# Performance work log

Hardware: AMD Instinct MI355X
Metric: run time of the kernel (lower is better)

Reference implementation:

```python
import jax, jax.numpy as jnp
import numpy as np

EPS = 1e-5
GROUPS = 8

def group_norm(x, gamma, beta):
    # x: [B,C,H,W], 8 groups
    B, C, H, W = x.shape
    xg = x.reshape(B, GROUPS, C // GROUPS, H, W)
    mu = jnp.mean(xg, axis=(2, 3, 4), keepdims=True)
    var = jnp.mean((xg - mu) ** 2, axis=(2, 3, 4), keepdims=True)
    xn = ((xg - mu) * jax.lax.rsqrt(var + EPS)).reshape(B, C, H, W)
    return xn * gamma[None, :, None, None] + beta[None, :, None, None]

def setup_inputs() -> dict:
    key = jax.random.key(0)
    ks = jax.random.split(key, 7)
    B, C, H, W = 4, 256, 64, 64
    x = jax.random.normal(ks[0], (B, C, H, W), dtype=jnp.float32)
    gamma = jnp.ones((C,), dtype=jnp.float32)
    beta = jnp.zeros((C,), dtype=jnp.float32)
    s = 1.0 / np.sqrt(C)
    w_qkv = jax.random.normal(ks[1], (3 * C, C), dtype=jnp.float32) * s
    b_qkv = jnp.zeros((3 * C,), dtype=jnp.float32)
    w_proj = jax.random.normal(ks[2], (C, C), dtype=jnp.float32) * s
    b_proj = jnp.zeros((C,), dtype=jnp.float32)
    return {"x": x, "gamma": gamma, "beta": beta, "w_qkv": w_qkv,
            "b_qkv": b_qkv, "w_proj": w_proj, "b_proj": b_proj}

def reference(x, gamma, beta, w_qkv, b_qkv, w_proj, b_proj):
    B, C, H, W = x.shape
    N = H * W
    h = group_norm(x, gamma, beta)
    # 1x1 conv == per-pixel matmul
    qkv = jnp.einsum('bchw,oc->bohw', h, w_qkv) + b_qkv[None, :, None, None]
    q, k, v = jnp.split(qkv, 3, axis=1)  # each [B,C,H,W]
    q = q.reshape(B, C, N).transpose(0, 2, 1)   # [B,N,C]
    k = k.reshape(B, C, N)                      # [B,C,N]
    v = v.reshape(B, C, N).transpose(0, 2, 1)   # [B,N,C]
    attn = jax.nn.softmax(jnp.einsum('bnc,bcm->bnm', q, k) / jnp.sqrt(jnp.float32(C)), axis=-1)
    out = jnp.einsum('bnm,bmc->bnc', attn, v)   # [B,N,C]
    out = out.transpose(0, 2, 1).reshape(B, C, H, W)
    proj = jnp.einsum('bchw,oc->bohw', out, w_proj) + b_proj[None, :, None, None]
    return x + proj
```

## Files before the change

### kernel.cpp

```cpp
#include <hip/hip_runtime.h>
#include <hip/hip_bf16.h>
#include <math.h>

#define B 4
#define C 256
#define G 8
#define N 4096
#define EPSV 1e-5f
#define QSCALE 0.0901684400f
#define THR2 11.5416f

typedef __attribute__((ext_vector_type(8))) short short8;
typedef __attribute__((ext_vector_type(16))) float f32x16;
typedef unsigned short ushort_t;
typedef unsigned int uint_t;

__device__ __forceinline__ ushort_t f2bf(float f) {
    union { float f; uint_t u; } c; c.f = f;
    uint_t u = c.u;
    uint_t r = (u + 0x7FFFu + ((u >> 16) & 1u)) >> 16;
    return (ushort_t)r;
}
__device__ __forceinline__ float bf2f(ushort_t h) {
    union { uint_t u; float f; } c; c.u = ((uint_t)h) << 16;
    return c.f;
}
__device__ __forceinline__ uint_t pack2(float a, float b) {
    return (uint_t)f2bf(a) | ((uint_t)f2bf(b) << 16);
}
__device__ __forceinline__ uint_t cvtpk_bf16(float lo, float hi) {
    uint_t r;
    asm("v_cvt_pk_bf16_f32 %0, %1, %2" : "=v"(r) : "v"(lo), "v"(hi));
    return r;
}
__device__ __forceinline__ float fexp2(float x) {
    return __builtin_amdgcn_exp2f(x);
}
__device__ __forceinline__ void gl_lds16(const void* g, void* l) {
    __builtin_amdgcn_global_load_lds(
        (const __attribute__((address_space(1))) void*)g,
        (__attribute__((address_space(3))) void*)l, 16, 0, 0);
}

__global__ __launch_bounds__(256) void gn_wconv(const float* __restrict__ x,
        float* __restrict__ partials, const float* __restrict__ wq,
        const float* __restrict__ wp, ushort_t* __restrict__ wbf) {
    int blk = blockIdx.x;
    if (blk < 256) {
        int bg = blk >> 3;
        int part = blk & 7;
        const float4* xp4 = (const float4*)(x + (size_t)bg * (32 * N) + (size_t)part * (32 * N / 8));
        float s = 0.f, ss = 0.f;
        for (int i = threadIdx.x; i < 4096; i += 256) {
            float4 v = xp4[i];
            s  += v.x + v.y + v.z + v.w;
            ss += v.x*v.x + v.y*v.y + v.z*v.z + v.w*v.w;
        }
        __shared__ float rs[256], rss[256];
        rs[threadIdx.x] = s; rss[threadIdx.x] = ss;
        __syncthreads();
        for (int off = 128; off > 0; off >>= 1) {
            if (threadIdx.x < off) {
                rs[threadIdx.x]  += rs[threadIdx.x + off];
                rss[threadIdx.x] += rss[threadIdx.x + off];
            }
            __syncthreads();
        }
        if (threadIdx.x == 0) {
            partials[(bg*8 + part)*2]     = rs[0];
            partials[(bg*8 + part)*2 + 1] = rss[0];
        }
    } else {
        int idx = (blk - 256)*256 + threadIdx.x;
        #pragma unroll
        for (int p = 0; p < 4; p++) {
            int id = idx + p*16384;
            float4 v = (id < 49152) ? ((const float4*)wq)[id] : ((const float4*)wp)[id - 49152];
            uint2 pk; pk.x = pack2(v.x, v.y); pk.y = pack2(v.z, v.w);
            *(uint2*)&wbf[(size_t)id*4] = pk;
        }
    }
}

__global__ __launch_bounds__(256) void qkv_fused(const float* __restrict__ x,
        const ushort_t* __restrict__ wbf, const float* __restrict__ gamma,
        const float* __restrict__ beta, const float* __restrict__ partials,
        const float* __restrict__ bias,
        ushort_t* __restrict__ qbf, ushort_t* __restrict__ kimg, ushort_t* __restrict__ vimg) {
    int b = blockIdx.z, o0 = blockIdx.y*64, n0 = blockIdx.x*128;
    int tid = threadIdx.x;
    int w = tid>>6, l = tid&63, l31 = l&31, lh = l>>5;
    int cg = tid >> 5;
    int nq = tid & 31;
    __shared__ short Ws[2][4096];
    __shared__ short Hs[2][8192];
    __shared__ float sst[16];

    if (tid < 8) {
        float s = 0.f, ss = 0.f;
        #pragma unroll
        for (int p = 0; p < 8; p++) {
            s  += partials[((b*8 + tid)*8 + p)*2];
            ss += partials[((b*8 + tid)*8 + p)*2 + 1];
        }
        const float inv = 1.f / 131072.f;
        float mu = s * inv;
        float var = fmaxf(ss * inv - mu*mu, 0.f);
        sst[tid*2]     = mu;
        sst[tid*2 + 1] = rsqrtf(var + EPSV);
    }
    __syncthreads();

    const ushort_t* wb = wbf + (size_t)o0*256;

    auto stageW = [&](int bb, int c0) {
        #pragma unroll
        for (int q = 0; q < 2; q++) {
            int u0 = q*256 + w*64;
            int u  = u0 + l;
            int row = u & 63, ch = u >> 6;
            gl_lds16(wb + (size_t)row*256 + c0 + ch*8, &Ws[bb][u0*8]);
        }
    };
    auto loadX = [&](int c0, float4* xv) {
        const float* xb = x + ((size_t)b*C + c0 + cg*8)*N + n0 + nq*4;
        #pragma unroll
        for (int e = 0; e < 8; e++)
            xv[e] = *(const float4*)(xb + (size_t)e*N);
    };
    auto writeH = [&](int bb, int c0, const float4* xv) {
        int cbase = c0 + cg*8;
        int g = cbase >> 5;
        float mu = sst[g*2], rs = sst[g*2+1];
        float ga[8], be[8];
        #pragma unroll
        for (int e = 0; e < 8; e++) {
            float gm = gamma[cbase+e];
            ga[e] = gm*rs;
            be[e] = beta[cbase+e] - mu*ga[e];
        }
        #pragma unroll
        for (int j = 0; j < 4; j++) {
            float h[8];
            #pragma unroll
            for (int e = 0; e < 8; e++) {
                float vx = (j==0) ? xv[e].x : (j==1) ? xv[e].y : (j==2) ? xv[e].z : xv[e].w;
                h[e] = vx*ga[e] + be[e];
            }
            uint4 pk;
            pk.x = pack2(h[0], h[1]);
            pk.y = pack2(h[2], h[3]);
            pk.z = pack2(h[4], h[5]);
            pk.w = pack2(h[6], h[7]);
            *(uint4*)&Hs[bb][(size_t)(cg*128 + nq*4 + j)*8] = pk;
        }
    };

    int wo = w & 1;
    int wn = w >> 1;
    f32x16 acc[2];
    #pragma unroll
    for (int nf = 0; nf < 2; nf++)
        #pragma unroll
        for (int r = 0; r < 16; r++) acc[nf][r] = 0.f;

    float4 xv[8];
    loadX(0, xv);
    stageW(0, 0);
    writeH(0, 0, xv);
    __syncthreads();

    for (int t = 0; t < 4; t++) {
        int bb = t & 1;
        if (t < 3) { stageW(bb^1, (t+1)*64); loadX((t+1)*64, xv); }
        short8 af[4];
        #pragma unroll
        for (int s = 0; s < 4; s++)
            af[s] = *(const short8*)&Ws[bb][((2*s+lh)*64 + wo*32 + l31)*8];
        #pragma unroll
        for (int nf = 0; nf < 2; nf++) {
            int nfr = wn*2 + nf;
            #pragma unroll
            for (int s = 0; s < 4; s++) {
                short8 hf = *(const short8*)&Hs[bb][((2*s+lh)*128 + nfr*32 + l31)*8];
                acc[nf] = __builtin_amdgcn_mfma_f32_32x32x16_bf16(af[s], hf, acc[nf], 0, 0, 0);
            }
        }
        if (t < 3) writeH(bb^1, (t+1)*64, xv);
        __syncthreads();
    }

    int ow = o0 + wo*32;
    float bv[16];
    #pragma unroll
    for (int r = 0; r < 16; r++) bv[r] = bias[ow + (r&3) + 8*(r>>2) + 4*lh];

    if (ow < 256) {
        #pragma unroll
        for (int nf = 0; nf < 2; nf++) {
            int n = n0 + (wn*2 + nf)*32 + l31;
            ushort_t* row = qbf + ((size_t)(b*N + n))*256 + ow;
            #pragma unroll
            for (int rp = 0; rp < 8; rp++) {
                int r0 = rp*2;
                int cl = (r0&3) + 8*(r0>>2) + 4*lh;
                uint_t wd = cvtpk_bf16((acc[nf][r0]+bv[r0])*QSCALE, (acc[nf][r0+1]+bv[r0+1])*QSCALE);
                *(uint_t*)(row + cl) = wd;
            }
        }
    } else if (ow < 512) {
        int cb = ow - 256;
        #pragma unroll
        for (int nf = 0; nf < 2; nf++) {
            int n = n0 + (wn*2 + nf)*32 + l31;
            ushort_t* tbase = kimg + (size_t)b*1048576 + (size_t)(n>>5)*8192
                            + (size_t)l31*8 + 4*lh;
            #pragma unroll
            for (int g = 0; g < 4; g++) {
                uint2 pk;
                pk.x = pack2(acc[nf][g*4+0]+bv[g*4+0], acc[nf][g*4+1]+bv[g*4+1]);
                pk.y = pack2(acc[nf][g*4+2]+bv[g*4+2], acc[nf][g*4+3]+bv[g*4+3]);
                *(uint2*)(tbase + (size_t)((cb>>3)+g)*256) = pk;
            }
        }
    } else {
        int cb = ow - 512;
        #pragma unroll
        for (int nf = 0; nf < 2; nf++) {
            int n = n0 + (wn*2 + nf)*32 + l31;
            ushort_t* tbase = vimg + (size_t)b*1048576 + (size_t)(n>>5)*8192
                            + (size_t)(l31>>3)*2048 + (l31&7);
            #pragma unroll
            for (int r = 0; r < 16; r++) {
                int cl = (r&3) + 8*(r>>2) + 4*lh;
                tbase[(size_t)(cb+cl)*8] = f2bf(acc[nf][r] + bv[r]);
            }
        }
    }
}

__global__ __launch_bounds__(256, 2) void attn_mfma(const ushort_t* __restrict__ qbf,
        const ushort_t* __restrict__ kimg, const ushort_t* __restrict__ vimg,
        ushort_t* __restrict__ part, float* __restrict__ ml) {
    int f = blockIdx.x;
    int comb = f & 15;
    int qt  = f >> 4;
    int b   = comb >> 2;
    int kvq = comb & 3;
    constexpr int NT = 32;
    int w = threadIdx.x >> 6;
    int l = threadIdx.x & 63;
    int l31 = l & 31, lh = l >> 5;

    __shared__ short KV[2][2][8192];

    int qbase = qt*128 + w*32;
    short8 qf[16];
    {
        const ushort_t* qrow = qbf + ((size_t)(b*N + qbase + l31))*256;
        #pragma unroll
        for (int s = 0; s < 16; s++)
            qf[s] = *(const short8*)(qrow + s*16 + lh*8);
    }

    f32x16 ot[8];
    #pragma unroll
    for (int mc = 0; mc < 8; mc++)
        #pragma unroll
        for (int r = 0; r < 16; r++) ot[mc][r] = 0.f;
    float m = -INFINITY, lsum = 0.f;

    const char* kbase = (const char*)kimg + (size_t)b*2097152;
    const char* vbase = (const char*)vimg + (size_t)b*2097152;

    auto stage = [&](int slot, int t) {
        int tile = kvq*32 + t;
        const char* kt = kbase + (size_t)tile*16384;
        const char* vt = vbase + (size_t)tile*16384;
        #pragma unroll
        for (int q = 0; q < 4; q++) {
            int u0 = (w*4 + q)*64;
            gl_lds16(kt + (u0 + l)*16, &KV[slot][0][u0*8]);
            gl_lds16(vt + (u0 + l)*16, &KV[slot][1][u0*8]);
        }
    };

    stage(0, 0);

    for (int t = 0; t < NT; t++) {
        int slot = t & 1;
        __syncthreads();
        if (t+1 < NT) stage(slot^1, t+1);

        f32x16 st0, st1;
        #pragma unroll
        for (int r = 0; r < 16; r++) { st0[r] = 0.f; st1[r] = 0.f; }
        const short* kb_ = &KV[slot][0][0];
        __builtin_amdgcn_s_setprio(1);
        #pragma unroll
        for (int s = 0; s < 8; s++) {
            short8 ka = *(const short8*)(kb_ + ((size_t)((4*s   + lh)*32 + l31))*8);
            short8 kc = *(const short8*)(kb_ + ((size_t)((4*s+2 + lh)*32 + l31))*8);
            st0 = __builtin_amdgcn_mfma_f32_32x32x16_bf16(ka, qf[2*s],   st0, 0, 0, 0);
            st1 = __builtin_amdgcn_mfma_f32_32x32x16_bf16(kc, qf[2*s+1], st1, 0, 0, 0);
        }
        __builtin_amdgcn_s_setprio(0);

        float sv[16];
        #pragma unroll
        for (int r = 0; r < 16; r++) sv[r] = st0[r] + st1[r];

        float a0 = fmaxf(sv[0], sv[1]),  a1 = fmaxf(sv[2], sv[3]);
        float a2 = fmaxf(sv[4], sv[5]),  a3 = fmaxf(sv[6], sv[7]);
        float a4 = fmaxf(sv[8], sv[9]),  a5 = fmaxf(sv[10], sv[11]);
        float a6 = fmaxf(sv[12], sv[13]), a7 = fmaxf(sv[14], sv[15]);
        float b0 = fmaxf(a0, a1), b1 = fmaxf(a2, a3), b2 = fmaxf(a4, a5), b3 = fmaxf(a6, a7);
        float pmax = fmaxf(fmaxf(b0, b1), fmaxf(b2, b3));
        pmax = fmaxf(pmax, __shfl_xor(pmax, 32));
        if (!__all(pmax <= m + THR2)) {
            float mn = fmaxf(m, pmax);
            float fac = fexp2(m - mn);
            m = mn;
            lsum *= fac;
            #pragma unroll
            for (int mc = 0; mc < 8; mc++)
                #pragma unroll
                for (int r = 0; r < 16; r++) ot[mc][r] *= fac;
        }
        float p[16];
        #pragma unroll
        for (int r = 0; r < 16; r++) p[r] = fexp2(sv[r] - m);
        float s0_ = (p[0]+p[1]) + (p[2]+p[3]);
        float s1_ = (p[4]+p[5]) + (p[6]+p[7]);
        float s2_ = (p[8]+p[9]) + (p[10]+p[11]);
        float s3_ = (p[12]+p[13]) + (p[14]+p[15]);
        float ls = (s0_+s1_) + (s2_+s3_);
        ls += __shfl_xor(ls, 32);
        lsum += ls;

        short8 pf0, pf1;
        {
            uint_t x0 = cvtpk_bf16(p[0], p[1]);
            uint_t y0 = cvtpk_bf16(p[4], p[5]);
            uint_t x1 = cvtpk_bf16(p[2], p[3]);
            uint_t y1 = cvtpk_bf16(p[6], p[7]);
            auto r0 = __builtin_amdgcn_permlane32_swap(x0, y0, false, false);
            auto r1 = __builtin_amdgcn_permlane32_swap(x1, y1, false, false);
            union { uint_t u[4]; short8 s8; } u_;
            u_.u[0] = r0[0]; u_.u[1] = r1[0]; u_.u[2] = r0[1]; u_.u[3] = r1[1];
            pf0 = u_.s8;
            uint_t x2 = cvtpk_bf16(p[8],  p[9]);
            uint_t y2 = cvtpk_bf16(p[12], p[13]);
            uint_t x3 = cvtpk_bf16(p[10], p[11]);
            uint_t y3 = cvtpk_bf16(p[14], p[15]);
            auto r2 = __builtin_amdgcn_permlane32_swap(x2, y2, false, false);
            auto r3 = __builtin_amdgcn_permlane32_swap(x3, y3, false, false);
            union { uint_t u[4]; short8 s8; } u2_;
            u2_.u[0] = r2[0]; u2_.u[1] = r3[0]; u2_.u[2] = r2[1]; u2_.u[3] = r3[1];
            pf1 = u2_.s8;
        }

        const short* vb_ = &KV[slot][1][0];
        __builtin_amdgcn_s_setprio(1);
        #pragma unroll
        for (int mc = 0; mc < 8; mc++) {
            short8 v0 = *(const short8*)(vb_ + ((size_t)((lh)*256   + mc*32 + l31))*8);
            short8 v1 = *(const short8*)(vb_ + ((size_t)((2+lh)*256 + mc*32 + l31))*8);
            ot[mc] = __builtin_amdgcn_mfma_f32_32x32x16_bf16(v0, pf0, ot[mc], 0, 0, 0);
            ot[mc] = __builtin_amdgcn_mfma_f32_32x32x16_bf16(v1, pf1, ot[mc], 0, 0, 0);
        }
        __builtin_amdgcn_s_setprio(0);
    }

    float invl = 1.f / lsum;
    ushort_t* pbase = part + (size_t)kvq*4194304 + ((size_t)(b*N + qbase + l31))*256;
    #pragma unroll
    for (int mc = 0; mc < 8; mc++)
        #pragma unroll
        for (int rp = 0; rp < 8; rp++) {
            int r0 = rp*2;
            uint_t wd = cvtpk_bf16(ot[mc][r0]*invl, ot[mc][r0+1]*invl);
            int c0 = (r0 & 3) + 8*(r0 >> 2) + 4*lh + 32*mc;
            *(uint_t*)(pbase + c0) = wd;
        }
    if (l < 32) {
        size_t row = (size_t)kvq*16384 + b*4096 + qbase + l;
        ml[row*2]     = m;
        ml[row*2 + 1] = lsum;
    }
}

__global__ __launch_bounds__(256) void proj_merge(const ushort_t* __restrict__ part,
        const float* __restrict__ ml, const ushort_t* __restrict__ wpbf,
        const float* __restrict__ bp, const float* __restrict__ x, float* __restrict__ out) {
    int b = blockIdx.z, o0 = blockIdx.y*128, n0 = blockIdx.x*64;
    int tid = threadIdx.x;
    int w = tid>>6, l = tid&63, l31 = l&31, lh = l>>5;
    __shared__ short Ws[2][8192];
    __shared__ short Hs[2][4096];

    const ushort_t* wb = wpbf + (size_t)o0*256;

    int srow = tid & 63;
    int ch0  = tid >> 6;
    size_t rowbase = ((size_t)(b*4096 + n0 + srow))*256;
    float wv[4];
    {
        float mv[4], lv[4];
        #pragma unroll
        for (int i = 0; i < 4; i++) {
            size_t rr = (size_t)i*16384 + b*4096 + n0 + srow;
            mv[i] = ml[rr*2];
            lv[i] = ml[rr*2 + 1];
        }
        float M = fmaxf(fmaxf(mv[0], mv[1]), fmaxf(mv[2], mv[3]));
        float wsum = 0.f;
        #pragma unroll
        for (int i = 0; i < 4; i++) { wv[i] = fexp2(mv[i] - M)*lv[i]; wsum += wv[i]; }
        float inv = 1.f / wsum;
        #pragma unroll
        for (int i = 0; i < 4; i++) wv[i] *= inv;
    }

    auto stageW = [&](int bb, int c0) {
        #pragma unroll
        for (int q = 0; q < 4; q++) {
            int u0 = (q*4 + w)*64;
            int u  = u0 + l;
            int row = u & 127, ch = u >> 7;
            gl_lds16(wb + (size_t)row*256 + c0 + ch*8, &Ws[bb][u0*8]);
        }
    };
    short8 hA[4], hB[4];
    auto Hload = [&](int c0) {
        #pragma unroll
        for (int i = 0; i < 4; i++) {
            const ushort_t* pp = part + (size_t)i*4194304 + rowbase + c0;
            hA[i] = *(const short8*)(pp + ch0*8);
            hB[i] = *(const short8*)(pp + (ch0+4)*8);
        }
    };
    auto Hwrite = [&](int bb) {
        float oA[8], oB[8];
        #pragma unroll
        for (int e = 0; e < 8; e++) { oA[e] = 0.f; oB[e] = 0.f; }
        #pragma unroll
        for (int i = 0; i < 4; i++) {
            float wi = wv[i];
            #pragma unroll
            for (int e = 0; e < 8; e++) {
                oA[e] += wi*bf2f((ushort_t)hA[i][e]);
                oB[e] += wi*bf2f((ushort_t)hB[i][e]);
            }
        }
        uint4 pkA, pkB;
        pkA.x = pack2(oA[0], oA[1]); pkA.y = pack2(oA[2], oA[3]);
        pkA.z = pack2(oA[4], oA[5]); pkA.w = pack2(oA[6], oA[7]);
        pkB.x = pack2(oB[0], oB[1]); pkB.y = pack2(oB[2], oB[3]);
        pkB.z = pack2(oB[4], oB[5]); pkB.w = pack2(oB[6], oB[7]);
        *(uint4*)&Hs[bb][(size_t)(ch0*64 + srow)*8]     = pkA;
        *(uint4*)&Hs[bb][(size_t)((ch0+4)*64 + srow)*8] = pkB;
    };

    f32x16 acc[2];
    #pragma unroll
    for (int nf = 0; nf < 2; nf++)
        #pragma unroll
        for (int r = 0; r < 16; r++) acc[nf][r] = 0.f;

    stageW(0, 0);
    Hload(0);
    Hwrite(0);
    __syncthreads();
    for (int t = 0; t < 4; t++) {
        int bb = t & 1;
        if (t < 3) { stageW(bb^1, (t+1)*64); Hload((t+1)*64); }
        short8 af[4];
        #pragma unroll
        for (int s = 0; s < 4; s++)
            af[s] = *(const short8*)&Ws[bb][((2*s+lh)*128 + w*32 + l31)*8];
        #pragma unroll
        for (int nf = 0; nf < 2; nf++) {
            #pragma unroll
            for (int s = 0; s < 4; s++) {
                short8 hf = *(const short8*)&Hs[bb][((2*s+lh)*64 + nf*32 + l31)*8];
                acc[nf] = __builtin_amdgcn_mfma_f32_32x32x16_bf16(af[s], hf, acc[nf], 0, 0, 0);
            }
        }
        if (t < 3) Hwrite(bb^1);
        __syncthreads();
    }

    int cw = o0 + w*32;
    float bv[16];
    #pragma unroll
    for (int r = 0; r < 16; r++) bv[r] = bp[cw + (r&3) + 8*(r>>2) + 4*lh];

    #pragma unroll
    for (int nf = 0; nf < 2; nf++) {
        int n = n0 + nf*32 + l31;
        #pragma unroll
        for (int r = 0; r < 16; r++) {
            int cl = (r&3) + 8*(r>>2) + 4*lh;
            size_t a = ((size_t)b*C + cw + cl)*N + n;
            out[a] = acc[nf][r] + bv[r] + x[a];
        }
    }
}

extern "C" void kernel_launch(void* const* d_in, const int* in_sizes, int n_in,
                              void* d_out, int out_size, void* d_ws, size_t ws_size,
                              hipStream_t stream) {
    const float* x      = (const float*)d_in[0];
    const float* gamma  = (const float*)d_in[1];
    const float* beta   = (const float*)d_in[2];
    const float* w_qkv  = (const float*)d_in[3];
    const float* b_qkv  = (const float*)d_in[4];
    const float* w_proj = (const float*)d_in[5];
    const float* b_proj = (const float*)d_in[6];
    float* out = (float*)d_out;
    char* wsb  = (char*)d_ws;

    const size_t MB = 1048576;
    ushort_t* qbf  = (ushort_t*)(wsb);
    ushort_t* kimg = (ushort_t*)(wsb + 8*MB);
    ushort_t* vimg = (ushort_t*)(wsb + 16*MB);
    ushort_t* part = (ushort_t*)(wsb + 24*MB);
    float*    ml   = (float*)  (wsb + 56*MB);
    float* partials = (float*) (wsb + 56*MB + 524288);
    ushort_t* wbf  = (ushort_t*)(wsb + 56*MB + 528384);

    gn_wconv<<<dim3(320), dim3(256), 0, stream>>>(x, partials, w_qkv, w_proj, wbf);
    qkv_fused<<<dim3(32, 12, 4), dim3(256), 0, stream>>>(x, wbf, gamma, beta, partials, b_qkv, qbf, kimg, vimg);
    attn_mfma<<<dim3(512), dim3(256), 0, stream>>>(qbf, kimg, vimg, part, ml);
    proj_merge<<<dim3(64, 2, 4), dim3(256), 0, stream>>>(part, ml, wbf + 196608, b_proj, x, out);
}
```

Before: 137.7 us.

## Software-pipeline attention: issue next QK^T before softmax, triple-buffer V

Restructures the flash-attention loop so the QK^T MFMAs for tile t+1 are issued right after the PV MFMAs of tile t. The softmax of tile t+1 then overlaps with matrix work, and K/V loads are prefetched two tiles ahead. LDS is split into a double-buffered K and a triple-buffered V, and the separate p[] array is folded into sv[] to save registers. This raises LDS use per block and may increase register pressure under launch_bounds(256,2). The new barrier placement also needs the buffer indexing to stay race-free.

```diff
diff --git a/kernel.cpp b/kernel.cpp
--- a/kernel.cpp
+++ b/kernel.cpp
@@ -252,7 +252,8 @@
     int l = threadIdx.x & 63;
     int l31 = l & 31, lh = l >> 5;
 
-    __shared__ short KV[2][2][8192];
+    __shared__ short Kl[2][8192];
+    __shared__ short Vl[3][8192];
 
     int qbase = qt*128 + w*32;
     short8 qf[16];
@@ -273,29 +274,25 @@
     const char* kbase = (const char*)kimg + (size_t)b*2097152;
     const char* vbase = (const char*)vimg + (size_t)b*2097152;
 
-    auto stage = [&](int slot, int t) {
-        int tile = kvq*32 + t;
+    auto stage = [&](int j) {
+        int tile = kvq*32 + j;
         const char* kt = kbase + (size_t)tile*16384;
         const char* vt = vbase + (size_t)tile*16384;
+        short* kd = &Kl[j & 1][0];
+        short* vd = &Vl[j % 3][0];
         #pragma unroll
         for (int q = 0; q < 4; q++) {
             int u0 = (w*4 + q)*64;
-            gl_lds16(kt + (u0 + l)*16, &KV[slot][0][u0*8]);
-            gl_lds16(vt + (u0 + l)*16, &KV[slot][1][u0*8]);
-        }
-    };
-
-    stage(0, 0);
-
-    for (int t = 0; t < NT; t++) {
-        int slot = t & 1;
-        __syncthreads();
-        if (t+1 < NT) stage(slot^1, t+1);
-
-        f32x16 st0, st1;
+            gl_lds16(kt + (u0 + l)*16, kd + u0*8);
+            gl_lds16(vt + (u0 + l)*16, vd + u0*8);
+        }
+    };
+
+    f32x16 st0, st1;
+    auto qk_issue = [&](int j) {
         #pragma unroll
         for (int r = 0; r < 16; r++) { st0[r] = 0.f; st1[r] = 0.f; }
-        const short* kb_ = &KV[slot][0][0];
+        const short* kb_ = &Kl[j & 1][0];
         __builtin_amdgcn_s_setprio(1);
         #pragma unroll
         for (int s = 0; s < 8; s++) {
@@ -305,7 +302,15 @@
             st1 = __builtin_amdgcn_mfma_f32_32x32x16_bf16(kc, qf[2*s+1], st1, 0, 0, 0);
         }
         __builtin_amdgcn_s_setprio(0);
-
+    };
+
+    stage(0);
+    __syncthreads();
+    qk_issue(0);
+    stage(1);
+    __syncthreads();
+
+    for (int t = 0; t < NT; t++) {
         float sv[16];
         #pragma unroll
         for (int r = 0; r < 16; r++) sv[r] = st0[r] + st1[r];
@@ -327,32 +332,31 @@
                 #pragma unroll
                 for (int r = 0; r < 16; r++) ot[mc][r] *= fac;
         }
-        float p[16];
-        #pragma unroll
-        for (int r = 0; r < 16; r++) p[r] = fexp2(sv[r] - m);
-        float s0_ = (p[0]+p[1]) + (p[2]+p[3]);
-        float s1_ = (p[4]+p[5]) + (p[6]+p[7]);
-        float s2_ = (p[8]+p[9]) + (p[10]+p[11]);
-        float s3_ = (p[12]+p[13]) + (p[14]+p[15]);
+        #pragma unroll
+        for (int r = 0; r < 16; r++) sv[r] = fexp2(sv[r] - m);
+        float s0_ = (sv[0]+sv[1]) + (sv[2]+sv[3]);
+        float s1_ = (sv[4]+sv[5]) + (sv[6]+sv[7]);
+        float s2_ = (sv[8]+sv[9]) + (sv[10]+sv[11]);
+        float s3_ = (sv[12]+sv[13]) + (sv[14]+sv[15]);
         float ls = (s0_+s1_) + (s2_+s3_);
         ls += __shfl_xor(ls, 32);
         lsum += ls;
 
         short8 pf0, pf1;
         {
-            uint_t x0 = cvtpk_bf16(p[0], p[1]);
-            uint_t y0 = cvtpk_bf16(p[4], p[5]);
-            uint_t x1 = cvtpk_bf16(p[2], p[3]);
-            uint_t y1 = cvtpk_bf16(p[6], p[7]);
+            uint_t x0 = cvtpk_bf16(sv[0], sv[1]);
+            uint_t y0 = cvtpk_bf16(sv[4], sv[5]);
+            uint_t x1 = cvtpk_bf16(sv[2], sv[3]);
+            uint_t y1 = cvtpk_bf16(sv[6], sv[7]);
             auto r0 = __builtin_amdgcn_permlane32_swap(x0, y0, false, false);
             auto r1 = __builtin_amdgcn_permlane32_swap(x1, y1, false, false);
             union { uint_t u[4]; short8 s8; } u_;
             u_.u[0] = r0[0]; u_.u[1] = r1[0]; u_.u[2] = r0[1]; u_.u[3] = r1[1];
             pf0 = u_.s8;
-            uint_t x2 = cvtpk_bf16(p[8],  p[9]);
-            uint_t y2 = cvtpk_bf16(p[12], p[13]);
-            uint_t x3 = cvtpk_bf16(p[10], p[11]);
-            uint_t y3 = cvtpk_bf16(p[14], p[15]);
+            uint_t x2 = cvtpk_bf16(sv[8],  sv[9]);
+            uint_t y2 = cvtpk_bf16(sv[12], sv[13]);
+            uint_t x3 = cvtpk_bf16(sv[10], sv[11]);
+            uint_t y3 = cvtpk_bf16(sv[14], sv[15]);
             auto r2 = __builtin_amdgcn_permlane32_swap(x2, y2, false, false);
             auto r3 = __builtin_amdgcn_permlane32_swap(x3, y3, false, false);
             union { uint_t u[4]; short8 s8; } u2_;
@@ -360,7 +364,7 @@
             pf1 = u2_.s8;
         }
 
-        const short* vb_ = &KV[slot][1][0];
+        const short* vb_ = &Vl[t % 3][0];
         __builtin_amdgcn_s_setprio(1);
         #pragma unroll
         for (int mc = 0; mc < 8; mc++) {
@@ -370,6 +374,10 @@
             ot[mc] = __builtin_amdgcn_mfma_f32_32x32x16_bf16(v1, pf1, ot[mc], 0, 0, 0);
         }
         __builtin_amdgcn_s_setprio(0);
+
+        if (t+1 < NT) qk_issue(t+1);
+        if (t+2 < NT) stage(t+2);
+        __syncthreads();
     }
 
     float invl = 1.f / lsum;
```

Result: no change. 138.2 us, median of 2 (+0.4%).
